# Optimization experiments

Measured on AMD Instinct MI355X. Metric: run time of the kernel, lower is better.

Reference implementation:

```python
import jax, jax.numpy as jnp
import numpy as np

B, V = 8, 400
D_MODEL, D_STATE, N_LAYERS = 256, 64, 2
D_INNER, DT_RANK, K_CONV = 512, 16, 4


def _silu(z):
    return z * jax.nn.sigmoid(z)


def _layernorm(z, w, b, eps=1e-5):
    mu = jnp.mean(z, axis=-1, keepdims=True)
    var = jnp.mean((z - mu) ** 2, axis=-1, keepdims=True)
    return (z - mu) * jax.lax.rsqrt(var + eps) * w + b


def _ssm_block(x, lw, lb, iw, ib, cw, cb, xw, dw, db, alog, dpar, ow, ob):
    # x: (N, L, D_MODEL). Mamba-style selective SSM block.
    N, L, _ = x.shape
    res = x
    xn = _layernorm(x, lw, lb)
    xr = xn @ iw + ib                      # (N, L, 2*D_INNER)
    xs, gate = jnp.split(xr, 2, axis=-1)   # each (N, L, D_INNER)
    # causal depthwise conv over L (kernel K_CONV)
    rhs = cw[:, None, :]                   # (K, 1, D_INNER)
    xc = jax.lax.conv_general_dilated(
        xs, rhs, window_strides=(1,), padding=[(K_CONV - 1, 0)],
        dimension_numbers=("NWC", "WIO", "NWC"), feature_group_count=D_INNER) + cb
    xc = _silu(xc)
    # input-dependent dt, B, C
    dbl = xc @ xw                          # (N, L, DT_RANK + 2*D_STATE)
    dt = dbl[..., :DT_RANK]
    Bm = dbl[..., DT_RANK:DT_RANK + D_STATE]
    Cm = dbl[..., DT_RANK + D_STATE:]
    dt = jax.nn.softplus(dt @ dw + db)     # (N, L, D_INNER)
    A = -jnp.exp(alog)                     # (D_INNER, D_STATE)
    dA = jnp.exp(jnp.einsum("nld,ds->nlds", dt, A))       # discretized A
    dBx = jnp.einsum("nld,nls,nld->nlds", dt, Bm, xc)      # discretized B*x

    def step(h, inp):
        dA_t, dBx_t, C_t = inp
        h = dA_t * h + dBx_t               # (N, D_INNER, D_STATE)
        y = jnp.einsum("nds,ns->nd", h, C_t)
        return h, y

    h0 = jnp.zeros((N, D_INNER, D_STATE), x.dtype)
    _, ys = jax.lax.scan(step, h0, (dA.transpose(1, 0, 2, 3),
                                    dBx.transpose(1, 0, 2, 3),
                                    Cm.transpose(1, 0, 2)))
    y = ys.transpose(1, 0, 2)              # (N, L, D_INNER)
    y = y + dpar * xc
    y = y * _silu(gate)
    return y @ ow + ob + res


def setup_inputs():
    key = jax.random.key(0)
    ks = jax.random.split(key, 8)
    f32 = jnp.float32

    def rn(k, shape, scale=0.02):
        return jax.random.normal(k, shape, dtype=f32) * scale

    return {
        "x": jax.random.normal(ks[0], (B, V, D_MODEL), dtype=f32),
        "ln_w": jnp.ones((N_LAYERS, D_MODEL), f32),
        "ln_b": jnp.zeros((N_LAYERS, D_MODEL), f32),
        "in_w": rn(ks[1], (N_LAYERS, D_MODEL, 2 * D_INNER)),
        "in_b": jnp.zeros((N_LAYERS, 2 * D_INNER), f32),
        "conv_w": rn(ks[2], (N_LAYERS, K_CONV, D_INNER), 0.1),
        "conv_b": jnp.zeros((N_LAYERS, D_INNER), f32),
        "xproj_w": rn(ks[3], (N_LAYERS, D_INNER, DT_RANK + 2 * D_STATE)),
        "dtproj_w": rn(ks[4], (N_LAYERS, DT_RANK, D_INNER)),
        "dtproj_b": rn(ks[5], (N_LAYERS, D_INNER), 0.1),
        "A_log": jnp.log(jnp.tile(jnp.arange(1, D_STATE + 1, dtype=f32)[None, None, :],
                                  (N_LAYERS, D_INNER, 1))),
        "D_param": jnp.ones((N_LAYERS, D_INNER), f32),
        "out_w": rn(ks[6], (N_LAYERS, D_INNER, D_MODEL)),
        "out_b": jnp.zeros((N_LAYERS, D_MODEL), f32),
    }


def reference(x, ln_w, ln_b, in_w, in_b, conv_w, conv_b, xproj_w, dtproj_w,
              dtproj_b, A_log, D_param, out_w, out_b):
    b, v, s = x.shape
    # seq_len == d_model, so the dynamically-created Linear branch is skipped
    h = x.reshape(b * v, 1, s)
    for i in range(N_LAYERS):
        h = _ssm_block(h, ln_w[i], ln_b[i], in_w[i], in_b[i], conv_w[i],
                       conv_b[i], xproj_w[i], dtproj_w[i], dtproj_b[i],
                       A_log[i], D_param[i], out_w[i], out_b[i])
    return h.reshape(b, v, D_MODEL)
```

## Files before the change

### kernel.cpp

```cpp
#include <hip/hip_runtime.h>
#include <math.h>


#define NTOK 3200
#define DM   256
#define DI   512
#define NX   1024
#define DTR  16
#define DS   64
#define NPJ  144
#define TPB  16
#define THR  512

#define PK1 (64*8*64*8)
#define PK2 (9*16*64*8)
#define PK3 (16*16*64*8)
#define PK4 (32*64*8)

using short8 = __attribute__((ext_vector_type(8))) short;
using f32x4  = __attribute__((ext_vector_type(4))) float;

__device__ __forceinline__ float siluf(float x){
    return x * __builtin_amdgcn_rcpf(1.0f + __expf(-x));
}
__device__ __forceinline__ float softplusf(float x){
    return (x > 15.f) ? x : __logf(1.0f + __expf(x));
}

__device__ __forceinline__ unsigned short f2bf(float f){
    unsigned int u = __float_as_uint(f);
    u += 0x7FFFu + ((u>>16)&1u);
    return (unsigned short)(u>>16);
}
__device__ __forceinline__ float bf2f(unsigned short h){
    return __uint_as_float(((unsigned int)h)<<16);
}
__device__ __forceinline__ int apos(int m, int k){
    return (((k>>5)*64) + (m&15) + (((k&31)>>3)<<4))*8 + (k&7);
}

__global__ __launch_bounds__(256) void prep_kernel(
    const float* __restrict__ in_w, const float* __restrict__ xw,
    const float* __restrict__ ow,   const float* __restrict__ dtw,
    unsigned short* __restrict__ ws)
{
    const int gid  = blockIdx.x*256 + threadIdx.x;
    const int lane = gid & 63;
    const int fr   = (gid>>6) % 944;
    const int l    = (gid>>6) / 944;
    unsigned short* W1p = ws;
    unsigned short* W2p = ws + 2*PK1;
    unsigned short* W3p = ws + 2*PK1 + 2*PK2;
    unsigned short* W4p = ws + 2*PK1 + 2*PK2 + 2*PK3;

    if (fr >= 912){
        const int nf = fr - 912;
        const float* src = dtw + (size_t)l*DTR*DI;
        const int n = nf*16 + (lane&15);
        short8 v;
        #pragma unroll
        for (int j=0;j<8;j++){
            const int k = (lane>>4)*8 + j;
            v[j] = (k < DTR) ? (short)f2bf(src[(size_t)k*DI + n]) : (short)0;
        }
        *(short8*)(W4p + (size_t)l*PK4 + ((size_t)nf*64 + lane)*8) = v;
        return;
    }
    const float* src; unsigned short* dst; int N, nf, ks;
    if (fr < 512){
        src = in_w + (size_t)l*DM*NX; N = NX; nf = fr>>3; ks = fr&7;
        dst = W1p + (size_t)l*PK1 + ((size_t)fr*64 + lane)*8;
    } else if (fr < 656){
        const int f2 = fr-512;
        src = xw + (size_t)l*DI*NPJ; N = NPJ; nf = f2>>4; ks = f2&15;
        dst = W2p + (size_t)l*PK2 + ((size_t)f2*64 + lane)*8;
    } else {
        const int f3 = fr-656;
        src = ow + (size_t)l*DI*DM; N = DM; nf = f3>>4; ks = f3&15;
        dst = W3p + (size_t)l*PK3 + ((size_t)f3*64 + lane)*8;
    }
    const int k0 = ks*32 + (lane>>4)*8;
    const int n  = nf*16 + (lane&15);
    short8 v;
    #pragma unroll
    for (int j=0;j<8;j++) v[j] = (short)f2bf(src[(size_t)(k0+j)*N + n]);
    *(short8*)dst = v;
}

#define G1_LOAD(buf, g) { \
    _Pragma("unroll") \
    for (int i=0;i<8;i++){ \
        buf[i]   = *(const short8*)(W1l + (((size_t)(nf0+i)*8 + (2*(g)+0))*64 + lane)*8); \
        buf[8+i] = *(const short8*)(W1l + (((size_t)(nf0+i)*8 + (2*(g)+1))*64 + lane)*8); \
    } }
#define G1_MFMA(buf, g) { \
    _Pragma("unroll") \
    for (int i=0;i<8;i++) \
        acc[i] = __builtin_amdgcn_mfma_f32_16x16x32_bf16(areg[2*(g)+0], buf[i], acc[i], 0,0,0); \
    _Pragma("unroll") \
    for (int i=0;i<8;i++) \
        acc[i] = __builtin_amdgcn_mfma_f32_16x16x32_bf16(areg[2*(g)+1], buf[8+i], acc[i], 0,0,0); \
    }

__global__ __launch_bounds__(THR)
__attribute__((amdgpu_waves_per_eu(2,2)))
void fused_net_kernel(
    const float* __restrict__ x,
    const float* __restrict__ ln_w, const float* __restrict__ ln_b,
    const float* __restrict__ in_b,
    const float* __restrict__ cw,   const float* __restrict__ cb,
    const float* __restrict__ dtb,
    const float* __restrict__ Dp,   const float* __restrict__ ob,
    const unsigned short* __restrict__ wsp,
    float* __restrict__ outp)
{
    __shared__ __align__(16) float h[TPB][DM+4];
    __shared__ __align__(16) unsigned short xnp[8*64*8];
    __shared__ __align__(16) unsigned short xcp[16*64*8];
    __shared__ __align__(16) unsigned short sgs[TPB][DI];
    __shared__ float dbl[TPB][NPJ+4];
    __shared__ float bcs[TPB];

    const int tid  = threadIdx.x;
    const int lane = tid & 63;
    const int wv   = tid >> 6;
    const int t0   = blockIdx.x * TPB;

    const unsigned short* W1p = wsp;
    const unsigned short* W2p = wsp + 2*PK1;
    const unsigned short* W3p = wsp + 2*PK1 + 2*PK2;
    const unsigned short* W4p = wsp + 2*PK1 + 2*PK2 + 2*PK3;

    #pragma unroll
    for (int i=0;i<2;i++){
        const int f4 = tid + i*THR;
        const int t = f4>>6, c4 = f4&63;
        *(float4*)&h[t][c4*4] = *(const float4*)(x + (size_t)(t0+t)*DM + c4*4);
    }
    __syncthreads();

    for (int l=0; l<2; ++l){
        const float* lwl = ln_w + l*DM;
        const float* lbl = ln_b + l*DM;
        const float* b1  = in_b + l*NX;
        const float* cw3 = cw + l*4*DI + 3*DI;
        const float* cbv = cb + l*DI;
        const float* bdl = dtb + l*DI;
        const float* Dl  = Dp + l*DI;
        const float* b3  = ob + l*DM;
        const unsigned short* W1l = W1p + (size_t)l*PK1;
        const unsigned short* W2l = W2p + (size_t)l*PK2;
        const unsigned short* W3l = W3p + (size_t)l*PK3;
        const unsigned short* W4l = W4p + (size_t)l*PK4;

        {
            const int t = tid>>5, q = tid&31, c0 = q*8;
            float4 v0 = *(float4*)&h[t][c0];
            float4 v1 = *(float4*)&h[t][c0+4];
            float s = v0.x+v0.y+v0.z+v0.w + v1.x+v1.y+v1.z+v1.w;
            #pragma unroll
            for (int o=16;o>=1;o>>=1) s += __shfl_xor(s, o, 32);
            const float mu = s*(1.0f/DM);
            float a[8] = {v0.x-mu,v0.y-mu,v0.z-mu,v0.w-mu,
                          v1.x-mu,v1.y-mu,v1.z-mu,v1.w-mu};
            float q2 = 0.f;
            #pragma unroll
            for (int i=0;i<8;i++) q2 += a[i]*a[i];
            #pragma unroll
            for (int o=16;o>=1;o>>=1) q2 += __shfl_xor(q2, o, 32);
            const float r = rsqrtf(q2*(1.0f/DM)+1e-5f);
            #pragma unroll
            for (int i=0;i<8;i++){
                const int c = c0+i;
                xnp[apos(t,c)] = f2bf(a[i]*r*lwl[c] + lbl[c]);
            }
        }
        __syncthreads();

        {
            const int nf0 = wv*8;
            const bool isx = (nf0 < 32);
            float b1v[8], cwv[8], cbb[8];
            #pragma unroll
            for (int i=0;i<8;i++){
                const int col = (nf0+i)*16 + (lane&15);
                b1v[i] = b1[col];
                cwv[i] = isx ? cw3[col] : 0.f;
                cbb[i] = isx ? cbv[col] : 0.f;
            }
            short8 areg[8];
            #pragma unroll
            for (int ks=0;ks<8;ks++)
                areg[ks] = *(const short8*)&xnp[(ks*64+lane)*8];
            f32x4 acc[8];
            #pragma unroll
            for (int i=0;i<8;i++) acc[i] = f32x4{0.f,0.f,0.f,0.f};

            short8 bA[16], bB[16];
            G1_LOAD(bA, 0);
            G1_LOAD(bB, 1);
            G1_MFMA(bA, 0);
            G1_LOAD(bA, 2);
            G1_MFMA(bB, 1);
            G1_LOAD(bB, 3);
            G1_MFMA(bA, 2);
            G1_MFMA(bB, 3);

            #pragma unroll
            for (int i=0;i<8;i++){
                const int col = (nf0+i)*16 + (lane&15);
                if (isx){
                    #pragma unroll
                    for (int r=0;r<4;r++){
                        const int t = (lane>>4)*4 + r;
                        xcp[apos(t,col)] = f2bf(siluf((acc[i][r]+b1v[i])*cwv[i] + cbb[i]));
                    }
                } else {
                    #pragma unroll
                    for (int r=0;r<4;r++){
                        const int t = (lane>>4)*4 + r;
                        sgs[t][col-DI] = f2bf(siluf(acc[i][r]+b1v[i]));
                    }
                }
            }
        }
        __syncthreads();

        {
            short8 b16[16];
            #pragma unroll
            for (int ks=0;ks<16;ks++)
                b16[ks] = *(const short8*)(W2l + (((size_t)wv*16 + ks)*64 + lane)*8);
            short8 a16[16];
            #pragma unroll
            for (int ks=0;ks<16;ks++)
                a16[ks] = *(const short8*)&xcp[(ks*64+lane)*8];
            f32x4 acc = f32x4{0.f,0.f,0.f,0.f};
            #pragma unroll
            for (int ks=0;ks<16;ks++)
                acc = __builtin_amdgcn_mfma_f32_16x16x32_bf16(a16[ks], b16[ks], acc, 0,0,0);
            const int col = wv*16 + (lane&15);
            #pragma unroll
            for (int r=0;r<4;r++) dbl[(lane>>4)*4 + r][col] = acc[r];
            if (wv == 0){
                #pragma unroll
                for (int ks=0;ks<16;ks++)
                    b16[ks] = *(const short8*)(W2l + (((size_t)8*16 + ks)*64 + lane)*8);
                f32x4 acc2 = f32x4{0.f,0.f,0.f,0.f};
                #pragma unroll
                for (int ks=0;ks<16;ks++)
                    acc2 = __builtin_amdgcn_mfma_f32_16x16x32_bf16(a16[ks], b16[ks], acc2, 0,0,0);
                const int col2 = 128 + (lane&15);
                #pragma unroll
                for (int r=0;r<4;r++) dbl[(lane>>4)*4 + r][col2] = acc2[r];
            }
        }
        __syncthreads();

        if (tid < 256){
            const int t = tid>>4, s0 = (tid&15)*4;
            float p = 0.f;
            #pragma unroll
            for (int j=0;j<4;j++)
                p += dbl[t][DTR+s0+j]*dbl[t][DTR+DS+s0+j];
            #pragma unroll
            for (int o=8;o>=1;o>>=1) p += __shfl_xor(p, o, 16);
            if ((tid&15)==0) bcs[t] = p;
        }
        __syncthreads();

        {
            short8 bw[4];
            #pragma unroll
            for (int i=0;i<4;i++)
                bw[i] = *(const short8*)(W4l + ((size_t)(wv*4+i)*64 + lane)*8);
            short8 a;
            const int m = lane&15, kg = lane>>4;
            #pragma unroll
            for (int j=0;j<8;j++){
                const int k = kg*8 + j;
                a[j] = (k < DTR) ? (short)f2bf(dbl[m][k]) : (short)0;
            }
            #pragma unroll
            for (int i=0;i<4;i++){
                const int nf = wv*4 + i;
                f32x4 acc = f32x4{0.f,0.f,0.f,0.f};
                acc = __builtin_amdgcn_mfma_f32_16x16x32_bf16(a, bw[i], acc, 0,0,0);
                const int c = nf*16 + (lane&15);
                const float bdv = bdl[c], Dv = Dl[c];
                #pragma unroll
                for (int r=0;r<4;r++){
                    const int t = kg*4 + r;
                    const float dtv = softplusf(acc[r] + bdv);
                    const int ip = apos(t,c);
                    const float yv = bf2f(xcp[ip])*(dtv*bcs[t] + Dv)*bf2f(sgs[t][c]);
                    xcp[ip] = f2bf(yv);
                }
            }
        }
        __syncthreads();

        {
            const int nf0 = wv*2;
            short8 b16a[16];
            #pragma unroll
            for (int ks=0;ks<16;ks++)
                b16a[ks] = *(const short8*)(W3l + (((size_t)nf0*16 + ks)*64 + lane)*8);
            short8 a16[16];
            #pragma unroll
            for (int ks=0;ks<16;ks++)
                a16[ks] = *(const short8*)&xcp[(ks*64+lane)*8];
            f32x4 acc0 = f32x4{0.f,0.f,0.f,0.f};
            #pragma unroll
            for (int ks=0;ks<16;ks++)
                acc0 = __builtin_amdgcn_mfma_f32_16x16x32_bf16(a16[ks], b16a[ks], acc0, 0,0,0);
            #pragma unroll
            for (int ks=0;ks<16;ks++)
                b16a[ks] = *(const short8*)(W3l + (((size_t)(nf0+1)*16 + ks)*64 + lane)*8);
            f32x4 acc1 = f32x4{0.f,0.f,0.f,0.f};
            #pragma unroll
            for (int ks=0;ks<16;ks++)
                acc1 = __builtin_amdgcn_mfma_f32_16x16x32_bf16(a16[ks], b16a[ks], acc1, 0,0,0);
            #pragma unroll
            for (int ni=0;ni<2;ni++){
                const f32x4 acc = ni ? acc1 : acc0;
                const int col = (nf0+ni)*16 + (lane&15);
                const float bo = b3[col];
                #pragma unroll
                for (int r=0;r<4;r++){
                    const int t = (lane>>4)*4 + r;
                    h[t][col] = acc[r] + bo + h[t][col];
                }
            }
        }
        __syncthreads();
    }

    #pragma unroll
    for (int i=0;i<2;i++){
        const int f4 = tid + i*THR;
        const int t = f4>>6, c4 = f4&63;
        *(float4*)(outp + (size_t)(t0+t)*DM + c4*4) = *(float4*)&h[t][c4*4];
    }
}

extern "C" void kernel_launch(void* const* d_in, const int* in_sizes, int n_in,
                              void* d_out, int out_size, void* d_ws, size_t ws_size,
                              hipStream_t stream)
{
    const float* x    = (const float*)d_in[0];
    const float* ln_w = (const float*)d_in[1];
    const float* ln_b = (const float*)d_in[2];
    const float* in_w = (const float*)d_in[3];
    const float* in_b = (const float*)d_in[4];
    const float* cw   = (const float*)d_in[5];
    const float* cb   = (const float*)d_in[6];
    const float* xw   = (const float*)d_in[7];
    const float* dtw  = (const float*)d_in[8];
    const float* dtb  = (const float*)d_in[9];
    const float* Dp   = (const float*)d_in[11];
    const float* ow   = (const float*)d_in[12];
    const float* ob   = (const float*)d_in[13];
    float* outp = (float*)d_out;
    unsigned short* wsp = (unsigned short*)d_ws;

    prep_kernel<<<472, 256, 0, stream>>>(in_w, xw, ow, dtw, wsp);
    fused_net_kernel<<<NTOK/TPB, THR, 0, stream>>>(
        x, ln_w, ln_b, in_b, cw, cb, dtb, Dp, ob, wsp, outp);
}
```

Before: 43.80 us.

## Prefetch next-stage weights into registers and fold B·C reduction into dt stage

Weight fragments for the x-projection, dt-projection and first half of the out-projection GEMMs are now loaded into registers during the preceding stage, so global-load latency overlaps earlier MFMA work instead of stalling at each stage start. The separate B·C dot-product stage, with its shared bcs array and extra barrier, is replaced by a per-wave float4 reduction plus shuffles inside the dt stage. The cost is much higher register pressure under the fixed two-waves-per-EU bound, which risks spills, and every wave now redundantly recomputes the B·C dot product.

```diff
diff --git a/kernel.cpp b/kernel.cpp
--- a/kernel.cpp
+++ b/kernel.cpp
@@ -118,8 +118,7 @@
     __shared__ __align__(16) unsigned short xnp[8*64*8];
     __shared__ __align__(16) unsigned short xcp[16*64*8];
     __shared__ __align__(16) unsigned short sgs[TPB][DI];
-    __shared__ float dbl[TPB][NPJ+4];
-    __shared__ float bcs[TPB];
+    __shared__ __align__(16) float dbl[TPB][NPJ+4];
 
     const int tid  = threadIdx.x;
     const int lane = tid & 63;
@@ -177,6 +176,7 @@
         }
         __syncthreads();
 
+        short8 pf2[16];
         {
             const int nf0 = wv*8;
             const bool isx = (nf0 < 32);
@@ -204,6 +204,9 @@
             G1_MFMA(bB, 1);
             G1_LOAD(bB, 3);
             G1_MFMA(bA, 2);
+            #pragma unroll
+            for (int ks=0;ks<16;ks++)
+                pf2[ks] = *(const short8*)(W2l + (((size_t)wv*16 + ks)*64 + lane)*8);
             G1_MFMA(bB, 3);
 
             #pragma unroll
@@ -226,11 +229,8 @@
         }
         __syncthreads();
 
-        {
-            short8 b16[16];
-            #pragma unroll
-            for (int ks=0;ks<16;ks++)
-                b16[ks] = *(const short8*)(W2l + (((size_t)wv*16 + ks)*64 + lane)*8);
+        short8 pf4[4], pf3a[16];
+        {
             short8 a16[16];
             #pragma unroll
             for (int ks=0;ks<16;ks++)
@@ -238,11 +238,12 @@
             f32x4 acc = f32x4{0.f,0.f,0.f,0.f};
             #pragma unroll
             for (int ks=0;ks<16;ks++)
-                acc = __builtin_amdgcn_mfma_f32_16x16x32_bf16(a16[ks], b16[ks], acc, 0,0,0);
+                acc = __builtin_amdgcn_mfma_f32_16x16x32_bf16(a16[ks], pf2[ks], acc, 0,0,0);
             const int col = wv*16 + (lane&15);
             #pragma unroll
             for (int r=0;r<4;r++) dbl[(lane>>4)*4 + r][col] = acc[r];
             if (wv == 0){
+                short8 b16[16];
                 #pragma unroll
                 for (int ks=0;ks<16;ks++)
                     b16[ks] = *(const short8*)(W2l + (((size_t)8*16 + ks)*64 + lane)*8);
@@ -254,28 +255,32 @@
                 #pragma unroll
                 for (int r=0;r<4;r++) dbl[(lane>>4)*4 + r][col2] = acc2[r];
             }
-        }
-        __syncthreads();
-
-        if (tid < 256){
-            const int t = tid>>4, s0 = (tid&15)*4;
+            #pragma unroll
+            for (int i=0;i<4;i++)
+                pf4[i] = *(const short8*)(W4l + ((size_t)(wv*4+i)*64 + lane)*8);
+            #pragma unroll
+            for (int ks=0;ks<16;ks++)
+                pf3a[ks] = *(const short8*)(W3l + (((size_t)(wv*2)*16 + ks)*64 + lane)*8);
+        }
+        __syncthreads();
+
+        {
+            const int btok = lane>>2, bq = lane&3;
             float p = 0.f;
             #pragma unroll
-            for (int j=0;j<4;j++)
-                p += dbl[t][DTR+s0+j]*dbl[t][DTR+DS+s0+j];
-            #pragma unroll
-            for (int o=8;o>=1;o>>=1) p += __shfl_xor(p, o, 16);
-            if ((tid&15)==0) bcs[t] = p;
-        }
-        __syncthreads();
-
-        {
-            short8 bw[4];
-            #pragma unroll
-            for (int i=0;i<4;i++)
-                bw[i] = *(const short8*)(W4l + ((size_t)(wv*4+i)*64 + lane)*8);
+            for (int f=0; f<4; f++){
+                const float4 bv = *(const float4*)&dbl[btok][DTR + bq*16 + f*4];
+                const float4 cv = *(const float4*)&dbl[btok][DTR + DS + bq*16 + f*4];
+                p += bv.x*cv.x + bv.y*cv.y + bv.z*cv.z + bv.w*cv.w;
+            }
+            p += __shfl_xor(p, 1, 64);
+            p += __shfl_xor(p, 2, 64);
+            const int m = lane&15, kg = lane>>4;
+            float bct[4];
+            #pragma unroll
+            for (int r=0;r<4;r++) bct[r] = __shfl(p, kg*16 + r*4, 64);
+
             short8 a;
-            const int m = lane&15, kg = lane>>4;
             #pragma unroll
             for (int j=0;j<8;j++){
                 const int k = kg*8 + j;
@@ -285,7 +290,7 @@
             for (int i=0;i<4;i++){
                 const int nf = wv*4 + i;
                 f32x4 acc = f32x4{0.f,0.f,0.f,0.f};
-                acc = __builtin_amdgcn_mfma_f32_16x16x32_bf16(a, bw[i], acc, 0,0,0);
+                acc = __builtin_amdgcn_mfma_f32_16x16x32_bf16(a, pf4[i], acc, 0,0,0);
                 const int c = nf*16 + (lane&15);
                 const float bdv = bdl[c], Dv = Dl[c];
                 #pragma unroll
@@ -293,7 +298,7 @@
                     const int t = kg*4 + r;
                     const float dtv = softplusf(acc[r] + bdv);
                     const int ip = apos(t,c);
-                    const float yv = bf2f(xcp[ip])*(dtv*bcs[t] + Dv)*bf2f(sgs[t][c]);
+                    const float yv = bf2f(xcp[ip])*(dtv*bct[r] + Dv)*bf2f(sgs[t][c]);
                     xcp[ip] = f2bf(yv);
                 }
             }
@@ -302,25 +307,22 @@
 
         {
             const int nf0 = wv*2;
-            short8 b16a[16];
-            #pragma unroll
-            for (int ks=0;ks<16;ks++)
-                b16a[ks] = *(const short8*)(W3l + (((size_t)nf0*16 + ks)*64 + lane)*8);
             short8 a16[16];
             #pragma unroll
             for (int ks=0;ks<16;ks++)
                 a16[ks] = *(const short8*)&xcp[(ks*64+lane)*8];
+            short8 b16b[16];
+            #pragma unroll
+            for (int ks=0;ks<16;ks++)
+                b16b[ks] = *(const short8*)(W3l + (((size_t)(nf0+1)*16 + ks)*64 + lane)*8);
             f32x4 acc0 = f32x4{0.f,0.f,0.f,0.f};
             #pragma unroll
             for (int ks=0;ks<16;ks++)
-                acc0 = __builtin_amdgcn_mfma_f32_16x16x32_bf16(a16[ks], b16a[ks], acc0, 0,0,0);
-            #pragma unroll
-            for (int ks=0;ks<16;ks++)
-                b16a[ks] = *(const short8*)(W3l + (((size_t)(nf0+1)*16 + ks)*64 + lane)*8);
+                acc0 = __builtin_amdgcn_mfma_f32_16x16x32_bf16(a16[ks], pf3a[ks], acc0, 0,0,0);
             f32x4 acc1 = f32x4{0.f,0.f,0.f,0.f};
             #pragma unroll
             for (int ks=0;ks<16;ks++)
-                acc1 = __builtin_amdgcn_mfma_f32_16x16x32_bf16(a16[ks], b16a[ks], acc1, 0,0,0);
+                acc1 = __builtin_amdgcn_mfma_f32_16x16x32_bf16(a16[ks], b16b[ks], acc1, 0,0,0);
             #pragma unroll
             for (int ni=0;ni<2;ni++){
                 const f32x4 acc = ni ? acc1 : acc0;
```

Result: faster. 42.15 us (-3.8%).
